# Kernel tuning notes

Hardware: AMD Instinct MI355X
Metric: run time of the kernel (lower is better)

The kernel has to match this reference:

```python
import jax, jax.numpy as jnp
import numpy as np

D_MODEL = 512
D_STATE = 64
BATCH = 8
SEQ = 4096
LN_EPS = 1e-3  # keras LayerNormalization default epsilon


def setup_inputs() -> dict:
    key = jax.random.key(0)
    ks = jax.random.split(key, 16)
    dm, dn = D_MODEL, D_STATE
    s_dm = 1.0 / np.sqrt(dm)
    s_dn = 1.0 / np.sqrt(dn)
    return {
        "x": jax.random.normal(ks[0], (BATCH, SEQ, dm), dtype=jnp.float32),
        "ln_gamma": jnp.ones((dm,), jnp.float32),
        "ln_beta": jnp.zeros((dm,), jnp.float32),
        "W_in": jax.random.normal(ks[1], (dm, dm), jnp.float32) * s_dm,
        "b_in": jnp.zeros((dm,), jnp.float32),
        "W_xs": jax.random.normal(ks[2], (dm, dn), jnp.float32) * s_dm,
        "W_B": jax.random.normal(ks[3], (dm, dn), jnp.float32) * s_dm,
        "b_B": jnp.zeros((dn,), jnp.float32),
        "W_C": jax.random.normal(ks[4], (dm, dn), jnp.float32) * s_dm,
        "b_C": jnp.zeros((dn,), jnp.float32),
        "A_log": jax.random.uniform(ks[5], (dn,), jnp.float32, minval=-4.0, maxval=-1.0),
        "D": jnp.ones((dm,), jnp.float32),
        "W_s2o": jax.random.normal(ks[6], (dn, dm), jnp.float32) * s_dn,
        "W_out": jax.random.normal(ks[7], (dm, dm), jnp.float32) * s_dm,
        "b_out": jnp.zeros((dm,), jnp.float32),
    }


def reference(x, ln_gamma, ln_beta, W_in, b_in, W_xs, W_B, b_B, W_C, b_C,
              A_log, D, W_s2o, W_out, b_out):
    residual = x
    # LayerNorm
    mu = jnp.mean(x, axis=-1, keepdims=True)
    var = jnp.var(x, axis=-1, keepdims=True)
    xn = (x - mu) * jax.lax.rsqrt(var + LN_EPS) * ln_gamma + ln_beta
    # Projections (all per-timestep, batched as one GEMM)
    u = xn @ W_in + b_in                      # [B,S,Dm]
    Bm = u @ W_B + b_B                        # [B,S,N]
    Cm = u @ W_C + b_C                        # [B,S,N]
    xs = u @ W_xs                             # [B,S,N]
    A_bar = jnp.exp(-jnp.exp(A_log))          # [N]
    Bu = Bm * xs                              # [B,S,N] input to recurrence
    # Sequential selective scan over time (time-major)
    Bu_t = jnp.swapaxes(Bu, 0, 1)             # [S,B,N]
    C_t = jnp.swapaxes(Cm, 0, 1)              # [S,B,N]
    h0 = jnp.zeros((x.shape[0], A_log.shape[0]), dtype=x.dtype)

    def step(h, inp):
        bu, c = inp
        h = A_bar * h + bu
        return h, c * h

    _, ys = jax.lax.scan(step, h0, (Bu_t, C_t))  # ys: [S,B,N]
    ys = jnp.swapaxes(ys, 0, 1)                  # [B,S,N]
    # state_to_output is linear & time-invariant -> apply after the scan
    y = ys @ W_s2o + D * u                       # [B,S,Dm]
    y = y @ W_out + b_out
    return y + residual                          # dropout is identity at inference
```

## Files before the change

### kernel.cpp

```cpp
#include <hip/hip_runtime.h>
#include <cstddef>

typedef unsigned short u16;

constexpr int DM   = 512;
constexpr int DN   = 64;
constexpr int SEQL = 4096;
constexpr int CH   = 128;
constexpr int LCH  = SEQL / CH;

typedef __attribute__((ext_vector_type(8))) short bf16x8;
typedef __attribute__((ext_vector_type(4))) float f32x4;

__device__ inline u16 f2bf(float f) {
    unsigned int u = __float_as_uint(f);
    unsigned int r = u + 0x7FFFu + ((u >> 16) & 1u);
    return (u16)(r >> 16);
}
__device__ inline float bf2f(u16 h) {
    return __uint_as_float(((unsigned int)h) << 16);
}

__device__ inline void gload_lds16(const void* g, void* l) {
    __builtin_amdgcn_global_load_lds(
        (const __attribute__((address_space(1))) void*)g,
        (__attribute__((address_space(3))) void*)l, 16, 0, 0);
}

__global__ __launch_bounds__(256) void k_ln(const float* __restrict__ X,
                                            const float* __restrict__ gamma,
                                            const float* __restrict__ beta,
                                            u16* __restrict__ Xn) {
    const int lane = threadIdx.x & 63;
    const int w    = threadIdx.x >> 6;
    const size_t row = (size_t)blockIdx.x * 4 + w;
    const float* xr = X + row * DM;
    float4 v0 = *reinterpret_cast<const float4*>(&xr[lane * 8]);
    float4 v1 = *reinterpret_cast<const float4*>(&xr[lane * 8 + 4]);
    float s  = v0.x + v0.y + v0.z + v0.w + v1.x + v1.y + v1.z + v1.w;
    float s2 = v0.x*v0.x + v0.y*v0.y + v0.z*v0.z + v0.w*v0.w
             + v1.x*v1.x + v1.y*v1.y + v1.z*v1.z + v1.w*v1.w;
#pragma unroll
    for (int o = 32; o > 0; o >>= 1) {
        s  += __shfl_xor(s, o);
        s2 += __shfl_xor(s2, o);
    }
    const float mu = s * (1.0f / DM);
    const float rs = rsqrtf(s2 * (1.0f / DM) - mu * mu + 1e-3f);
    float4 g0 = *reinterpret_cast<const float4*>(&gamma[lane * 8]);
    float4 g1 = *reinterpret_cast<const float4*>(&gamma[lane * 8 + 4]);
    float4 b0 = *reinterpret_cast<const float4*>(&beta[lane * 8]);
    float4 b1 = *reinterpret_cast<const float4*>(&beta[lane * 8 + 4]);
    union { u16 h[8]; uint4 v; } pk;
    pk.h[0] = f2bf((v0.x - mu) * rs * g0.x + b0.x);
    pk.h[1] = f2bf((v0.y - mu) * rs * g0.y + b0.y);
    pk.h[2] = f2bf((v0.z - mu) * rs * g0.z + b0.z);
    pk.h[3] = f2bf((v0.w - mu) * rs * g0.w + b0.w);
    pk.h[4] = f2bf((v1.x - mu) * rs * g1.x + b1.x);
    pk.h[5] = f2bf((v1.y - mu) * rs * g1.y + b1.y);
    pk.h[6] = f2bf((v1.z - mu) * rs * g1.z + b1.z);
    pk.h[7] = f2bf((v1.w - mu) * rs * g1.w + b1.w);
    *reinterpret_cast<uint4*>(&Xn[row * DM + lane * 8]) = pk.v;
}

__global__ __launch_bounds__(256) void k_wtransG(const float* __restrict__ W,
                                                 u16* __restrict__ Wt,
                                                 int K, int N) {
    __shared__ float tile[64][65];
    const int bx = blockIdx.x, by = blockIdx.y;
    const int tx = threadIdx.x & 63, ty = threadIdx.x >> 6;
#pragma unroll
    for (int r = ty; r < 64; r += 4)
        tile[r][tx] = W[(size_t)(by * 64 + r) * N + bx * 64 + tx];
    __syncthreads();
#pragma unroll
    for (int r = ty; r < 64; r += 4)
        Wt[(size_t)(bx * 64 + r) * K + by * 64 + tx] = f2bf(tile[tx][r]);
}

template <int MODE>
__global__ __launch_bounds__(256) void k_mfma512(
    const u16* __restrict__ A, const u16* __restrict__ Bt,
    const float* __restrict__ bias, const float* __restrict__ resid,
    void* __restrict__ OutV)
{
    constexpr int BK = 32;
    __shared__ u16 As[128 * BK];
    __shared__ u16 Bs[128 * BK];
    const int tid  = threadIdx.x;
    const int lane = tid & 63;
    const int w    = tid >> 6;
    const int wr   = w >> 1, wc = w & 1;
    const int m0   = blockIdx.y * 128;
    const int n0   = blockIdx.x * 128;

    f32x4 acc[4][4];
#pragma unroll
    for (int i = 0; i < 4; i++)
#pragma unroll
      for (int j = 0; j < 4; j++) acc[i][j] = (f32x4){0.f, 0.f, 0.f, 0.f};

    const int srow = tid >> 2;
    const int sk   = (tid & 3) * 8;
    const u16* aptr0 = A  + (size_t)(m0 + srow) * DM + sk;
    const u16* aptr1 = aptr0 + (size_t)64 * DM;
    const u16* bptr0 = Bt + (size_t)(n0 + srow) * DM + sk;
    const u16* bptr1 = bptr0 + (size_t)64 * DM;
    u16* asB0 = As + w * 512;
    u16* asB1 = As + 2048 + w * 512;
    u16* bsB0 = Bs + w * 512;
    u16* bsB1 = Bs + 2048 + w * 512;

    const int kg = lane >> 4;
    const int lr = lane & 15;
    const int aoff = (wr * 64 + lr) * BK + kg * 8;
    const int boff = (wc * 64 + lr) * BK + kg * 8;

    for (int k0 = 0; k0 < DM; k0 += BK) {
        gload_lds16(aptr0, asB0);
        gload_lds16(aptr1, asB1);
        gload_lds16(bptr0, bsB0);
        gload_lds16(bptr1, bsB1);
        aptr0 += BK; aptr1 += BK; bptr0 += BK; bptr1 += BK;
        __syncthreads();
        bf16x8 af[4], bfr[4];
#pragma unroll
        for (int i = 0; i < 4; i++)
            af[i]  = *reinterpret_cast<const bf16x8*>(&As[aoff + i * 16 * BK]);
#pragma unroll
        for (int j = 0; j < 4; j++)
            bfr[j] = *reinterpret_cast<const bf16x8*>(&Bs[boff + j * 16 * BK]);
#pragma unroll
        for (int i = 0; i < 4; i++)
#pragma unroll
          for (int j = 0; j < 4; j++)
            acc[i][j] = __builtin_amdgcn_mfma_f32_16x16x32_bf16(af[i], bfr[j], acc[i][j], 0, 0, 0);
        __syncthreads();
    }

#pragma unroll
    for (int j = 0; j < 4; j++) {
        const int col = n0 + wc * 64 + j * 16 + lr;
        const float bv = bias[col];
#pragma unroll
        for (int i = 0; i < 4; i++) {
            const int rbase = m0 + wr * 64 + i * 16 + kg * 4;
#pragma unroll
            for (int r = 0; r < 4; r++) {
                const size_t idx = (size_t)(rbase + r) * DM + col;
                float v = acc[i][j][r] + bv;
                if (MODE == 0) {
                    ((u16*)OutV)[idx] = f2bf(v);
                } else {
                    ((float*)OutV)[idx] = v + resid[idx];
                }
            }
        }
    }
}

__global__ __launch_bounds__(256) void k_mfma_bcx(
    const u16* __restrict__ A, const u16* __restrict__ Bt,
    const float* __restrict__ bB, const float* __restrict__ bC,
    float* __restrict__ Bu, float* __restrict__ Cc)
{
    constexpr int BK = 32;
    __shared__ u16 As[64 * BK];
    __shared__ u16 Bs[192 * BK];
    const int tid  = threadIdx.x;
    const int lane = tid & 63;
    const int w    = tid >> 6;
    const int m0   = blockIdx.x * 64;

    f32x4 acc[12];
#pragma unroll
    for (int j = 0; j < 12; j++) acc[j] = (f32x4){0.f, 0.f, 0.f, 0.f};

    const int srow = tid >> 2;
    const int sk   = (tid & 3) * 8;
    const u16* aptr  = A  + (size_t)(m0 + srow) * DM + sk;
    const u16* bptr0 = Bt + (size_t)srow * DM + sk;
    const u16* bptr1 = bptr0 + (size_t)64 * DM;
    const u16* bptr2 = bptr0 + (size_t)128 * DM;
    u16* asB  = As + w * 512;
    u16* bsB0 = Bs + w * 512;
    u16* bsB1 = Bs + 2048 + w * 512;
    u16* bsB2 = Bs + 4096 + w * 512;

    const int kg = lane >> 4;
    const int lr = lane & 15;
    const int aoff = (w * 16 + lr) * BK + kg * 8;

    for (int k0 = 0; k0 < DM; k0 += BK) {
        gload_lds16(aptr,  asB);
        gload_lds16(bptr0, bsB0);
        gload_lds16(bptr1, bsB1);
        gload_lds16(bptr2, bsB2);
        aptr += BK; bptr0 += BK; bptr1 += BK; bptr2 += BK;
        __syncthreads();
        bf16x8 af = *reinterpret_cast<const bf16x8*>(&As[aoff]);
#pragma unroll
        for (int j = 0; j < 12; j++) {
            bf16x8 bfr = *reinterpret_cast<const bf16x8*>(&Bs[(j * 16 + lr) * BK + kg * 8]);
            acc[j] = __builtin_amdgcn_mfma_f32_16x16x32_bf16(af, bfr, acc[j], 0, 0, 0);
        }
        __syncthreads();
    }

#pragma unroll
    for (int j = 0; j < 4; j++) {
        const int col = j * 16 + lr;
        const float bBv = bB[col], bCv = bC[col];
#pragma unroll
        for (int r = 0; r < 4; r++) {
            const int grow = m0 + w * 16 + kg * 4 + r;
            const float xs = acc[j][r];
            const float bm = acc[j + 4][r] + bBv;
            const float cm = acc[j + 8][r] + bCv;
            Bu[(size_t)grow * DN + col] = bm * xs;
            Cc[(size_t)grow * DN + col] = cm;
        }
    }
}

__global__ void k_scan1(const float* __restrict__ Bu, const float* __restrict__ Alog,
                        float* __restrict__ Hl) {
    const int n = threadIdx.x;
    const int c = blockIdx.x;
    const int b = blockIdx.y;
    const float a = expf(-expf(Alog[n]));
    const float* p = Bu + ((size_t)(b * SEQL + c * LCH)) * DN + n;
    float h = 0.f;
#pragma unroll
    for (int t = 0; t < LCH; t++) h = fmaf(a, h, p[(size_t)t * DN]);
    Hl[(b * DN + n) * CH + c] = h;
}

__global__ void k_carry(const float* __restrict__ Hl, const float* __restrict__ Alog,
                        float* __restrict__ Hin) {
    const int i = threadIdx.x;
    const int n = i & 63;
    const float a  = expf(-expf(Alog[n]));
    const float aL = powf(a, (float)LCH);
    float hend = 0.f;
    for (int c = 0; c < CH; c++) {
        Hin[(size_t)i * CH + c] = hend;
        hend = fmaf(aL, hend, Hl[(size_t)i * CH + c]);
    }
}

__global__ void k_scan2(const float* __restrict__ Bu, const float* __restrict__ Cc,
                        const float* __restrict__ Hin, const float* __restrict__ Alog,
                        u16* __restrict__ Ysb) {
    const int n = threadIdx.x;
    const int c = blockIdx.x;
    const int b = blockIdx.y;
    const float a = expf(-expf(Alog[n]));
    float h = Hin[((size_t)(b * DN + n)) * CH + c];
    const size_t base = ((size_t)(b * SEQL + c * LCH)) * DN + n;
#pragma unroll
    for (int t = 0; t < LCH; t++) {
        h = fmaf(a, h, Bu[base + (size_t)t * DN]);
        Ysb[base + (size_t)t * DN] = f2bf(Cc[base + (size_t)t * DN] * h);
    }
}

__global__ __launch_bounds__(256) void k_mfma_s2o(
    const u16* __restrict__ A, const u16* __restrict__ Bt,
    const float* __restrict__ Dv, u16* __restrict__ UT)
{
    constexpr int BK = 32;
    __shared__ u16 As[128 * BK];
    __shared__ u16 Bs[128 * BK];
    const int tid  = threadIdx.x;
    const int lane = tid & 63;
    const int w    = tid >> 6;
    const int wr   = w >> 1, wc = w & 1;
    const int m0   = blockIdx.y * 128;
    const int n0   = blockIdx.x * 128;

    f32x4 acc[4][4];
#pragma unroll
    for (int i = 0; i < 4; i++)
#pragma unroll
      for (int j = 0; j < 4; j++) acc[i][j] = (f32x4){0.f, 0.f, 0.f, 0.f};

    const int srow = tid >> 2;
    const int sk   = (tid & 3) * 8;
    const u16* aptr0 = A  + (size_t)(m0 + srow) * DN + sk;
    const u16* aptr1 = aptr0 + (size_t)64 * DN;
    const u16* bptr0 = Bt + (size_t)(n0 + srow) * DN + sk;
    const u16* bptr1 = bptr0 + (size_t)64 * DN;
    u16* asB0 = As + w * 512;
    u16* asB1 = As + 2048 + w * 512;
    u16* bsB0 = Bs + w * 512;
    u16* bsB1 = Bs + 2048 + w * 512;

    const int kg = lane >> 4;
    const int lr = lane & 15;
    const int aoff = (wr * 64 + lr) * BK + kg * 8;
    const int boff = (wc * 64 + lr) * BK + kg * 8;

#pragma unroll
    for (int k0 = 0; k0 < DN; k0 += BK) {
        gload_lds16(aptr0, asB0);
        gload_lds16(aptr1, asB1);
        gload_lds16(bptr0, bsB0);
        gload_lds16(bptr1, bsB1);
        aptr0 += BK; aptr1 += BK; bptr0 += BK; bptr1 += BK;
        __syncthreads();
        bf16x8 af[4], bfr[4];
#pragma unroll
        for (int i = 0; i < 4; i++)
            af[i]  = *reinterpret_cast<const bf16x8*>(&As[aoff + i * 16 * BK]);
#pragma unroll
        for (int j = 0; j < 4; j++)
            bfr[j] = *reinterpret_cast<const bf16x8*>(&Bs[boff + j * 16 * BK]);
#pragma unroll
        for (int i = 0; i < 4; i++)
#pragma unroll
          for (int j = 0; j < 4; j++)
            acc[i][j] = __builtin_amdgcn_mfma_f32_16x16x32_bf16(af[i], bfr[j], acc[i][j], 0, 0, 0);
        __syncthreads();
    }

#pragma unroll
    for (int j = 0; j < 4; j++) {
        const int col = n0 + wc * 64 + j * 16 + lr;
        const float dv = Dv[col];
#pragma unroll
        for (int i = 0; i < 4; i++) {
            const int rbase = m0 + wr * 64 + i * 16 + kg * 4;
#pragma unroll
            for (int r = 0; r < 4; r++) {
                const size_t idx = (size_t)(rbase + r) * DM + col;
                const float u = bf2f(UT[idx]);
                UT[idx] = f2bf(acc[i][j][r] + dv * u);
            }
        }
    }
}

extern "C" void kernel_launch(void* const* d_in, const int* in_sizes, int n_in,
                              void* d_out, int out_size, void* d_ws, size_t ws_size,
                              hipStream_t stream) {
    const float* X     = (const float*)d_in[0];
    const float* gamma = (const float*)d_in[1];
    const float* beta  = (const float*)d_in[2];
    const float* W_in  = (const float*)d_in[3];
    const float* b_in  = (const float*)d_in[4];
    const float* W_xs  = (const float*)d_in[5];
    const float* W_B   = (const float*)d_in[6];
    const float* b_B   = (const float*)d_in[7];
    const float* W_C   = (const float*)d_in[8];
    const float* b_C   = (const float*)d_in[9];
    const float* A_log = (const float*)d_in[10];
    const float* Dv    = (const float*)d_in[11];
    const float* W_s2o = (const float*)d_in[12];
    const float* W_out = (const float*)d_in[13];
    const float* b_out = (const float*)d_in[14];
    float* out = (float*)d_out;

    const int M = in_sizes[0] / DM;
    const int B = M / SEQL;

    float* ws  = (float*)d_ws;
    float* Bu  = ws;
    float* Cc  = Bu + (size_t)M * DN;
    float* Hl  = Cc + (size_t)M * DN;
    float* Hin = Hl + (size_t)B * DN * CH;
    u16* Xn    = (u16*)(Hin + (size_t)B * DN * CH);
    u16* Ub    = Xn + (size_t)M * DM;
    u16* Ysb   = Ub + (size_t)M * DM;
    u16* WinT  = Ysb + (size_t)M * DN;
    u16* WoutT = WinT + (size_t)DM * DM;
    u16* WbcxT = WoutT + (size_t)DM * DM;
    u16* Ws2oT = WbcxT + (size_t)3 * DN * DM;

    k_ln<<<M / 4, 256, 0, stream>>>(X, gamma, beta, Xn);
    k_wtransG<<<dim3(8, 8), 256, 0, stream>>>(W_in,  WinT,  DM, DM);
    k_wtransG<<<dim3(8, 8), 256, 0, stream>>>(W_out, WoutT, DM, DM);
    k_wtransG<<<dim3(1, 8), 256, 0, stream>>>(W_xs, WbcxT,            DM, DN);
    k_wtransG<<<dim3(1, 8), 256, 0, stream>>>(W_B,  WbcxT + 64 * DM,  DM, DN);
    k_wtransG<<<dim3(1, 8), 256, 0, stream>>>(W_C,  WbcxT + 128 * DM, DM, DN);
    k_wtransG<<<dim3(8, 1), 256, 0, stream>>>(W_s2o, Ws2oT, DN, DM);

    k_mfma512<0><<<dim3(DM / 128, M / 128), 256, 0, stream>>>(Xn, WinT, b_in, nullptr, Ub);
    k_mfma_bcx<<<dim3(M / 64), 256, 0, stream>>>(Ub, WbcxT, b_B, b_C, Bu, Cc);
    k_scan1<<<dim3(CH, B), 64, 0, stream>>>(Bu, A_log, Hl);
    k_carry<<<1, B * DN, 0, stream>>>(Hl, A_log, Hin);
    k_scan2<<<dim3(CH, B), 64, 0, stream>>>(Bu, Cc, Hin, A_log, Ysb);
    k_mfma_s2o<<<dim3(DM / 128, M / 128), 256, 0, stream>>>(Ysb, Ws2oT, Dv, Ub);
    k_mfma512<1><<<dim3(DM / 128, M / 128), 256, 0, stream>>>(Ub, WoutT, b_out, X, out);
}
```

Measured before the change: 186.0 us.

## Fold s2o and D-skip into concatenated output GEMM and double-buffer LDS

Precomputes W_s2o@W_out and diag(D)·W_out into one concatenated bf16 weight (K=576), so the final output comes from a single GEMM over [ys | u] instead of a separate s2o GEMM plus a read-modify-write of u. It also double-buffers LDS staging in the GEMM kernels, overlapping the next tile's global-to-LDS load with the current tile's MFMAs, and remaps block IDs so consecutive blocks spread across XCDs. The product of the two weight matrices is rounded to bf16 once, which can change numerics slightly. The weight-product kernel is a naive per-thread 512-length dot product that runs inside the timed launch.

```diff
diff --git a/kernel.cpp b/kernel.cpp
--- a/kernel.cpp
+++ b/kernel.cpp
@@ -8,6 +8,7 @@
 constexpr int SEQL = 4096;
 constexpr int CH   = 128;
 constexpr int LCH  = SEQL / CH;
+constexpr int KC   = DM + DN;
 
 typedef __attribute__((ext_vector_type(8))) short bf16x8;
 typedef __attribute__((ext_vector_type(4))) float f32x4;
@@ -63,9 +64,10 @@
     *reinterpret_cast<uint4*>(&Xn[row * DM + lane * 8]) = pk.v;
 }
 
-__global__ __launch_bounds__(256) void k_wtransG(const float* __restrict__ W,
+__global__ __launch_bounds__(256) void k_wtransS(const float* __restrict__ W,
                                                  u16* __restrict__ Wt,
-                                                 int K, int N) {
+                                                 int K, int N, int ldo,
+                                                 const float* __restrict__ scale) {
     __shared__ float tile[64][65];
     const int bx = blockIdx.x, by = blockIdx.y;
     const int tx = threadIdx.x & 63, ty = threadIdx.x >> 6;
@@ -73,26 +75,47 @@
     for (int r = ty; r < 64; r += 4)
         tile[r][tx] = W[(size_t)(by * 64 + r) * N + bx * 64 + tx];
     __syncthreads();
+    const float sc = scale ? scale[by * 64 + tx] : 1.0f;
 #pragma unroll
     for (int r = ty; r < 64; r += 4)
-        Wt[(size_t)(bx * 64 + r) * K + by * 64 + tx] = f2bf(tile[tx][r]);
-}
-
-template <int MODE>
-__global__ __launch_bounds__(256) void k_mfma512(
-    const u16* __restrict__ A, const u16* __restrict__ Bt,
-    const float* __restrict__ bias, const float* __restrict__ resid,
-    void* __restrict__ OutV)
+        Wt[(size_t)(bx * 64 + r) * ldo + by * 64 + tx] = f2bf(sc * tile[tx][r]);
+}
+
+__global__ __launch_bounds__(256) void k_wcat(const float* __restrict__ Ws2o,
+                                              const float* __restrict__ Wout,
+                                              u16* __restrict__ Wcat) {
+    const int tn = threadIdx.x & 63;
+    const int tk = threadIdx.x >> 6;
+    const int n  = blockIdx.x * 64 + tn;
+    const int k  = blockIdx.y * 4 + tk;
+    float s = 0.f;
+#pragma unroll 8
+    for (int j = 0; j < DM; ++j)
+        s = fmaf(Ws2o[(size_t)k * DM + j], Wout[(size_t)j * DM + n], s);
+    Wcat[(size_t)n * KC + k] = f2bf(s);
+}
+
+__global__ __launch_bounds__(256) void k_g1(const u16* __restrict__ A,
+                                            const u16* __restrict__ Bt,
+                                            const float* __restrict__ bias,
+                                            u16* __restrict__ Out)
 {
-    constexpr int BK = 32;
-    __shared__ u16 As[128 * BK];
-    __shared__ u16 Bs[128 * BK];
-    const int tid  = threadIdx.x;
-    const int lane = tid & 63;
-    const int w    = tid >> 6;
-    const int wr   = w >> 1, wc = w & 1;
-    const int m0   = blockIdx.y * 128;
-    const int n0   = blockIdx.x * 128;
+    __shared__ u16 As[2][4096];
+    __shared__ u16 Bs[2][4096];
+    const int tid = threadIdx.x, lane = tid & 63, w = tid >> 6;
+    const int wr = w >> 1, wc = w & 1;
+    int lid = blockIdx.y * gridDim.x + blockIdx.x;
+    const int cpx = (gridDim.x * gridDim.y) >> 3;
+    lid = (lid & 7) * cpx + (lid >> 3);
+    const int n0 = (lid & 3) * 128;
+    const int m0 = (lid >> 2) * 128;
+
+    const int srow = tid >> 2, sk = (tid & 3) * 8;
+    const u16* aR = A  + (size_t)(m0 + srow) * DM + sk;
+    const u16* bR = Bt + (size_t)(n0 + srow) * DM + sk;
+    const int kg = lane >> 4, lr = lane & 15;
+    const int aoff = (wr * 64 + lr) * 32 + kg * 8;
+    const int boff = (wc * 64 + lr) * 32 + kg * 8;
 
     f32x4 acc[4][4];
 #pragma unroll
@@ -100,36 +123,27 @@
 #pragma unroll
       for (int j = 0; j < 4; j++) acc[i][j] = (f32x4){0.f, 0.f, 0.f, 0.f};
 
-    const int srow = tid >> 2;
-    const int sk   = (tid & 3) * 8;
-    const u16* aptr0 = A  + (size_t)(m0 + srow) * DM + sk;
-    const u16* aptr1 = aptr0 + (size_t)64 * DM;
-    const u16* bptr0 = Bt + (size_t)(n0 + srow) * DM + sk;
-    const u16* bptr1 = bptr0 + (size_t)64 * DM;
-    u16* asB0 = As + w * 512;
-    u16* asB1 = As + 2048 + w * 512;
-    u16* bsB0 = Bs + w * 512;
-    u16* bsB1 = Bs + 2048 + w * 512;
-
-    const int kg = lane >> 4;
-    const int lr = lane & 15;
-    const int aoff = (wr * 64 + lr) * BK + kg * 8;
-    const int boff = (wc * 64 + lr) * BK + kg * 8;
-
-    for (int k0 = 0; k0 < DM; k0 += BK) {
-        gload_lds16(aptr0, asB0);
-        gload_lds16(aptr1, asB1);
-        gload_lds16(bptr0, bsB0);
-        gload_lds16(bptr1, bsB1);
-        aptr0 += BK; aptr1 += BK; bptr0 += BK; bptr1 += BK;
-        __syncthreads();
+    auto STAGE = [&](int buf, int s) {
+        const u16* a0 = aR + s * 32;
+        const u16* b0 = bR + s * 32;
+        gload_lds16(a0,           &As[buf][w * 512]);
+        gload_lds16(a0 + 64 * DM, &As[buf][2048 + w * 512]);
+        gload_lds16(b0,           &Bs[buf][w * 512]);
+        gload_lds16(b0 + 64 * DM, &Bs[buf][2048 + w * 512]);
+    };
+
+    STAGE(0, 0);
+    __syncthreads();
+    for (int s = 0; s < 16; ++s) {
+        const int cur = s & 1;
+        if (s + 1 < 16) STAGE(cur ^ 1, s + 1);
         bf16x8 af[4], bfr[4];
 #pragma unroll
         for (int i = 0; i < 4; i++)
-            af[i]  = *reinterpret_cast<const bf16x8*>(&As[aoff + i * 16 * BK]);
+            af[i]  = *reinterpret_cast<const bf16x8*>(&As[cur][aoff + i * 512]);
 #pragma unroll
         for (int j = 0; j < 4; j++)
-            bfr[j] = *reinterpret_cast<const bf16x8*>(&Bs[boff + j * 16 * BK]);
+            bfr[j] = *reinterpret_cast<const bf16x8*>(&Bs[cur][boff + j * 512]);
 #pragma unroll
         for (int i = 0; i < 4; i++)
 #pragma unroll
@@ -146,15 +160,8 @@
         for (int i = 0; i < 4; i++) {
             const int rbase = m0 + wr * 64 + i * 16 + kg * 4;
 #pragma unroll
-            for (int r = 0; r < 4; r++) {
-                const size_t idx = (size_t)(rbase + r) * DM + col;
-                float v = acc[i][j][r] + bv;
-                if (MODE == 0) {
-                    ((u16*)OutV)[idx] = f2bf(v);
-                } else {
-                    ((float*)OutV)[idx] = v + resid[idx];
-                }
-            }
+            for (int r = 0; r < 4; r++)
+                Out[(size_t)(rbase + r) * DM + col] = f2bf(acc[i][j][r] + bv);
         }
     }
 }
@@ -164,44 +171,39 @@
     const float* __restrict__ bB, const float* __restrict__ bC,
     float* __restrict__ Bu, float* __restrict__ Cc)
 {
-    constexpr int BK = 32;
-    __shared__ u16 As[64 * BK];
-    __shared__ u16 Bs[192 * BK];
-    const int tid  = threadIdx.x;
-    const int lane = tid & 63;
-    const int w    = tid >> 6;
-    const int m0   = blockIdx.x * 64;
+    __shared__ u16 As[2][2048];
+    __shared__ u16 Bs[2][6144];
+    const int tid = threadIdx.x, lane = tid & 63, w = tid >> 6;
+    const int m0 = blockIdx.x * 64;
 
     f32x4 acc[12];
 #pragma unroll
     for (int j = 0; j < 12; j++) acc[j] = (f32x4){0.f, 0.f, 0.f, 0.f};
 
-    const int srow = tid >> 2;
-    const int sk   = (tid & 3) * 8;
-    const u16* aptr  = A  + (size_t)(m0 + srow) * DM + sk;
-    const u16* bptr0 = Bt + (size_t)srow * DM + sk;
-    const u16* bptr1 = bptr0 + (size_t)64 * DM;
-    const u16* bptr2 = bptr0 + (size_t)128 * DM;
-    u16* asB  = As + w * 512;
-    u16* bsB0 = Bs + w * 512;
-    u16* bsB1 = Bs + 2048 + w * 512;
-    u16* bsB2 = Bs + 4096 + w * 512;
-
-    const int kg = lane >> 4;
-    const int lr = lane & 15;
-    const int aoff = (w * 16 + lr) * BK + kg * 8;
-
-    for (int k0 = 0; k0 < DM; k0 += BK) {
-        gload_lds16(aptr,  asB);
-        gload_lds16(bptr0, bsB0);
-        gload_lds16(bptr1, bsB1);
-        gload_lds16(bptr2, bsB2);
-        aptr += BK; bptr0 += BK; bptr1 += BK; bptr2 += BK;
-        __syncthreads();
-        bf16x8 af = *reinterpret_cast<const bf16x8*>(&As[aoff]);
+    const int srow = tid >> 2, sk = (tid & 3) * 8;
+    const u16* aR = A  + (size_t)(m0 + srow) * DM + sk;
+    const u16* bR = Bt + (size_t)srow * DM + sk;
+    const int kg = lane >> 4, lr = lane & 15;
+    const int aoff = (w * 16 + lr) * 32 + kg * 8;
+
+    auto STAGE = [&](int buf, int s) {
+        const u16* a0 = aR + s * 32;
+        const u16* b0 = bR + s * 32;
+        gload_lds16(a0,            &As[buf][w * 512]);
+        gload_lds16(b0,            &Bs[buf][w * 512]);
+        gload_lds16(b0 + 64 * DM,  &Bs[buf][2048 + w * 512]);
+        gload_lds16(b0 + 128 * DM, &Bs[buf][4096 + w * 512]);
+    };
+
+    STAGE(0, 0);
+    __syncthreads();
+    for (int s = 0; s < 16; ++s) {
+        const int cur = s & 1;
+        if (s + 1 < 16) STAGE(cur ^ 1, s + 1);
+        bf16x8 af = *reinterpret_cast<const bf16x8*>(&As[cur][aoff]);
 #pragma unroll
         for (int j = 0; j < 12; j++) {
-            bf16x8 bfr = *reinterpret_cast<const bf16x8*>(&Bs[(j * 16 + lr) * BK + kg * 8]);
+            bf16x8 bfr = *reinterpret_cast<const bf16x8*>(&Bs[cur][(j * 16 + lr) * 32 + kg * 8]);
             acc[j] = __builtin_amdgcn_mfma_f32_16x16x32_bf16(af, bfr, acc[j], 0, 0, 0);
         }
         __syncthreads();
@@ -265,19 +267,28 @@
     }
 }
 
-__global__ __launch_bounds__(256) void k_mfma_s2o(
-    const u16* __restrict__ A, const u16* __restrict__ Bt,
-    const float* __restrict__ Dv, u16* __restrict__ UT)
+__global__ __launch_bounds__(256) void k_gfuse(
+    const u16* __restrict__ Ysb, const u16* __restrict__ Ub,
+    const u16* __restrict__ Wcat, const float* __restrict__ bias,
+    const float* __restrict__ X, float* __restrict__ Out)
 {
-    constexpr int BK = 32;
-    __shared__ u16 As[128 * BK];
-    __shared__ u16 Bs[128 * BK];
-    const int tid  = threadIdx.x;
-    const int lane = tid & 63;
-    const int w    = tid >> 6;
-    const int wr   = w >> 1, wc = w & 1;
-    const int m0   = blockIdx.y * 128;
-    const int n0   = blockIdx.x * 128;
+    __shared__ u16 As[2][4096];
+    __shared__ u16 Bs[2][4096];
+    const int tid = threadIdx.x, lane = tid & 63, w = tid >> 6;
+    const int wr = w >> 1, wc = w & 1;
+    int lid = blockIdx.y * gridDim.x + blockIdx.x;
+    const int cpx = (gridDim.x * gridDim.y) >> 3;
+    lid = (lid & 7) * cpx + (lid >> 3);
+    const int n0 = (lid & 3) * 128;
+    const int m0 = (lid >> 2) * 128;
+
+    const int srow = tid >> 2, sk = (tid & 3) * 8;
+    const u16* aY = Ysb + (size_t)(m0 + srow) * DN + sk;
+    const u16* aU = Ub  + (size_t)(m0 + srow) * DM + sk;
+    const u16* bR = Wcat + (size_t)(n0 + srow) * KC + sk;
+    const int kg = lane >> 4, lr = lane & 15;
+    const int aoff = (wr * 64 + lr) * 32 + kg * 8;
+    const int boff = (wc * 64 + lr) * 32 + kg * 8;
 
     f32x4 acc[4][4];
 #pragma unroll
@@ -285,37 +296,29 @@
 #pragma unroll
       for (int j = 0; j < 4; j++) acc[i][j] = (f32x4){0.f, 0.f, 0.f, 0.f};
 
-    const int srow = tid >> 2;
-    const int sk   = (tid & 3) * 8;
-    const u16* aptr0 = A  + (size_t)(m0 + srow) * DN + sk;
-    const u16* aptr1 = aptr0 + (size_t)64 * DN;
-    const u16* bptr0 = Bt + (size_t)(n0 + srow) * DN + sk;
-    const u16* bptr1 = bptr0 + (size_t)64 * DN;
-    u16* asB0 = As + w * 512;
-    u16* asB1 = As + 2048 + w * 512;
-    u16* bsB0 = Bs + w * 512;
-    u16* bsB1 = Bs + 2048 + w * 512;
-
-    const int kg = lane >> 4;
-    const int lr = lane & 15;
-    const int aoff = (wr * 64 + lr) * BK + kg * 8;
-    const int boff = (wc * 64 + lr) * BK + kg * 8;
-
-#pragma unroll
-    for (int k0 = 0; k0 < DN; k0 += BK) {
-        gload_lds16(aptr0, asB0);
-        gload_lds16(aptr1, asB1);
-        gload_lds16(bptr0, bsB0);
-        gload_lds16(bptr1, bsB1);
-        aptr0 += BK; aptr1 += BK; bptr0 += BK; bptr1 += BK;
-        __syncthreads();
+    auto STAGE = [&](int buf, int s) {
+        const u16 *a0, *a1;
+        if (s < 2) { a0 = aY + s * 32;       a1 = a0 + 64 * DN; }
+        else       { a0 = aU + (s - 2) * 32; a1 = a0 + 64 * DM; }
+        const u16* b0 = bR + s * 32;
+        gload_lds16(a0,           &As[buf][w * 512]);
+        gload_lds16(a1,           &As[buf][2048 + w * 512]);
+        gload_lds16(b0,           &Bs[buf][w * 512]);
+        gload_lds16(b0 + 64 * KC, &Bs[buf][2048 + w * 512]);
+    };
+
+    STAGE(0, 0);
+    __syncthreads();
+    for (int s = 0; s < 18; ++s) {
+        const int cur = s & 1;
+        if (s + 1 < 18) STAGE(cur ^ 1, s + 1);
         bf16x8 af[4], bfr[4];
 #pragma unroll
         for (int i = 0; i < 4; i++)
-            af[i]  = *reinterpret_cast<const bf16x8*>(&As[aoff + i * 16 * BK]);
+            af[i]  = *reinterpret_cast<const bf16x8*>(&As[cur][aoff + i * 512]);
 #pragma unroll
         for (int j = 0; j < 4; j++)
-            bfr[j] = *reinterpret_cast<const bf16x8*>(&Bs[boff + j * 16 * BK]);
+            bfr[j] = *reinterpret_cast<const bf16x8*>(&Bs[cur][boff + j * 512]);
 #pragma unroll
         for (int i = 0; i < 4; i++)
 #pragma unroll
@@ -327,15 +330,14 @@
 #pragma unroll
     for (int j = 0; j < 4; j++) {
         const int col = n0 + wc * 64 + j * 16 + lr;
-        const float dv = Dv[col];
+        const float bv = bias[col];
 #pragma unroll
         for (int i = 0; i < 4; i++) {
             const int rbase = m0 + wr * 64 + i * 16 + kg * 4;
 #pragma unroll
             for (int r = 0; r < 4; r++) {
                 const size_t idx = (size_t)(rbase + r) * DM + col;
-                const float u = bf2f(UT[idx]);
-                UT[idx] = f2bf(acc[i][j][r] + dv * u);
+                Out[idx] = acc[i][j][r] + bv + X[idx];
             }
         }
     }
@@ -373,23 +375,21 @@
     u16* Ub    = Xn + (size_t)M * DM;
     u16* Ysb   = Ub + (size_t)M * DM;
     u16* WinT  = Ysb + (size_t)M * DN;
-    u16* WoutT = WinT + (size_t)DM * DM;
-    u16* WbcxT = WoutT + (size_t)DM * DM;
-    u16* Ws2oT = WbcxT + (size_t)3 * DN * DM;
+    u16* WbcxT = WinT + (size_t)DM * DM;
+    u16* WcatT = WbcxT + (size_t)3 * DN * DM;
 
     k_ln<<<M / 4, 256, 0, stream>>>(X, gamma, beta, Xn);
-    k_wtransG<<<dim3(8, 8), 256, 0, stream>>>(W_in,  WinT,  DM, DM);
-    k_wtransG<<<dim3(8, 8), 256, 0, stream>>>(W_out, WoutT, DM, DM);
-    k_wtransG<<<dim3(1, 8), 256, 0, stream>>>(W_xs, WbcxT,            DM, DN);
-    k_wtransG<<<dim3(1, 8), 256, 0, stream>>>(W_B,  WbcxT + 64 * DM,  DM, DN);
-    k_wtransG<<<dim3(1, 8), 256, 0, stream>>>(W_C,  WbcxT + 128 * DM, DM, DN);
-    k_wtransG<<<dim3(8, 1), 256, 0, stream>>>(W_s2o, Ws2oT, DN, DM);
-
-    k_mfma512<0><<<dim3(DM / 128, M / 128), 256, 0, stream>>>(Xn, WinT, b_in, nullptr, Ub);
+    k_wtransS<<<dim3(8, 8), 256, 0, stream>>>(W_in, WinT, DM, DM, DM, nullptr);
+    k_wtransS<<<dim3(1, 8), 256, 0, stream>>>(W_xs, WbcxT,            DM, DN, DM, nullptr);
+    k_wtransS<<<dim3(1, 8), 256, 0, stream>>>(W_B,  WbcxT + 64 * DM,  DM, DN, DM, nullptr);
+    k_wtransS<<<dim3(1, 8), 256, 0, stream>>>(W_C,  WbcxT + 128 * DM, DM, DN, DM, nullptr);
+    k_wtransS<<<dim3(8, 8), 256, 0, stream>>>(W_out, WcatT + 64, DM, DM, KC, Dv);
+    k_wcat<<<dim3(8, 16), 256, 0, stream>>>(W_s2o, W_out, WcatT);
+
+    k_g1<<<dim3(4, M / 128), 256, 0, stream>>>(Xn, WinT, b_in, Ub);
     k_mfma_bcx<<<dim3(M / 64), 256, 0, stream>>>(Ub, WbcxT, b_B, b_C, Bu, Cc);
     k_scan1<<<dim3(CH, B), 64, 0, stream>>>(Bu, A_log, Hl);
     k_carry<<<1, B * DN, 0, stream>>>(Hl, A_log, Hin);
     k_scan2<<<dim3(CH, B), 64, 0, stream>>>(Bu, Cc, Hin, A_log, Ysb);
-    k_mfma_s2o<<<dim3(DM / 128, M / 128), 256, 0, stream>>>(Ysb, Ws2oT, Dv, Ub);
-    k_mfma512<1><<<dim3(DM / 128, M / 128), 256, 0, stream>>>(Ub, WoutT, b_out, X, out);
-}
+    k_gfuse<<<dim3(4, M / 128), 256, 0, stream>>>(Ysb, Ub, WcatT, b_out, X, out);
+}
```

Measured after the change: 174.1 us. 1.07x faster.
